# Performance work log

Measured on AMD Instinct MI355X. Metric: run time of the kernel, lower is better.

## Reference

```python
import jax, jax.numpy as jnp
import numpy as np

B, D, P = 8192, 256, 4096
TEMP = 0.5
MOMENTUM = 0.9
EPS = 1e-12  # matches torch F.normalize eps


def _l2_normalize(x):
    n = jnp.sqrt(jnp.sum(x * x, axis=1, keepdims=True))
    return x / jnp.maximum(n, EPS)


def setup_inputs() -> dict:
    key = jax.random.key(0)
    k1, k2, k3 = jax.random.split(key, 3)
    embeddings = jax.random.normal(k1, (B, D), dtype=jnp.float32)
    prototypes = jax.random.normal(k2, (P, D), dtype=jnp.float32)
    cluster_ids = jax.random.randint(k3, (B,), 0, P, dtype=jnp.int64)
    return {"embeddings": embeddings, "prototypes": prototypes, "cluster_ids": cluster_ids}


def reference(embeddings, prototypes, cluster_ids):
    cluster_ids = cluster_ids.astype(jnp.int32)
    emb_norm = _l2_normalize(embeddings)            # [B, D]
    proto_norm = _l2_normalize(prototypes)          # [P, D]
    sim = (emb_norm @ proto_norm.T) / TEMP          # [B, P]

    rows = jnp.arange(sim.shape[0])
    pos_sim = sim[rows, cluster_ids]                # [B]
    neg_sim = sim.at[rows, cluster_ids].set(-jnp.inf)
    # stable logsumexp over negatives (positive column masked out)
    max_val = jnp.max(neg_sim, axis=1, keepdims=True)
    lse = jnp.log(jnp.sum(jnp.exp(neg_sim - max_val), axis=1)) + max_val[:, 0]
    loss = jnp.mean(-pos_sim + lse)

    # serial per-sample EMA prototype update (faithful to the torch for-loop,
    # including sequential dependence on repeated cluster ids)
    def step(protos, xe):
        cid, e = xe
        new_row = MOMENTUM * protos[cid] + (1.0 - MOMENTUM) * e
        return protos.at[cid].set(new_row), None

    new_prototypes, _ = jax.lax.scan(step, prototypes, (cluster_ids, embeddings))
    return loss, new_prototypes
```

## Files before the change

kernel.cpp:

```cpp
#include <hip/hip_runtime.h>
#include <hip/hip_bf16.h>
#include <math.h>

#define Bn 8192
#define Dn 256
#define Pn 4096

#define SCALE 2.8853900817779268f
#define LN2   0.6931471805599453f

using f16x8 = _Float16 __attribute__((ext_vector_type(8)));
using f16x4 = _Float16 __attribute__((ext_vector_type(4)));
using f32x16 = float __attribute__((ext_vector_type(16)));

__global__ void norm_hist_kernel(const float* __restrict__ emb, const float* __restrict__ protos,
                                 const int* __restrict__ cid,
                                 _Float16* __restrict__ embn, _Float16* __restrict__ pron,
                                 float* __restrict__ s_glob, int* __restrict__ hist) {
    __shared__ int h[Pn];
    int gid  = blockIdx.x;
    bool do_hist = (gid < Bn / 256);
    if (do_hist)
        for (int c = threadIdx.x; c < Pn; c += 256) h[c] = 0;

    int row  = gid * 4 + (threadIdx.x >> 6);
    int lane = threadIdx.x & 63;
    const float* in;
    _Float16* out;
    int r;
    float post;
    if (row < Bn) { in = emb;    out = embn; r = row;      post = SCALE; }
    else          { in = protos; out = pron; r = row - Bn; post = 1.0f;  }
    const float4 v = reinterpret_cast<const float4*>(in + (size_t)r * Dn)[lane];
    float ss = v.x * v.x + v.y * v.y + v.z * v.z + v.w * v.w;
#pragma unroll
    for (int m = 1; m <= 32; m <<= 1) ss += __shfl_xor(ss, m);
    float scale = post / fmaxf(sqrtf(ss), 1e-12f);
    f16x4 o;
    o[0] = (_Float16)(v.x * scale);
    o[1] = (_Float16)(v.y * scale);
    o[2] = (_Float16)(v.z * scale);
    o[3] = (_Float16)(v.w * scale);
    reinterpret_cast<f16x4*>(out + (size_t)r * Dn)[lane] = o;

    if (gid < 32) s_glob[gid * 256 + threadIdx.x] = 0.0f;

    if (do_hist) {
        __syncthreads();
        atomicAdd(&h[cid[gid * 256 + threadIdx.x]], 1);
        __syncthreads();
        for (int c = threadIdx.x; c < Pn; c += 256)
            hist[gid * Pn + c] = h[c];
    }
}

__global__ __launch_bounds__(256, 2)
void gemm_expsum_kernel(const _Float16* __restrict__ embn, const _Float16* __restrict__ pron,
                        float* __restrict__ s_glob) {
    __shared__ _Float16 Bs[2][32 * Dn];
    const int w    = threadIdx.x >> 6;
    const int lane = threadIdx.x & 63;
    const int lo   = lane & 31;
    const int hi   = lane >> 5;
    const int rbase = blockIdx.x * 128 + w * 32;
    const int cbase = blockIdx.y * 256;

    const _Float16* ap = embn + (size_t)(rbase + lo) * Dn + hi * 8;
    f16x8 a[16];
#pragma unroll
    for (int kk = 0; kk < 16; ++kk)
        a[kk] = *reinterpret_cast<const f16x8*>(ap + kk * 16);

    float s[16];
#pragma unroll
    for (int r = 0; r < 16; ++r) s[r] = 0.0f;

    auto stage = [&](int sub, _Float16* buf) {
#pragma unroll
        for (int i = 0; i < 4; ++i) {
            int g = i * 4 + w;
            const _Float16* gsrc =
                pron + (size_t)(cbase + sub * 32 + lo) * Dn + g * 16 + hi * 8;
            char* l = (char*)buf + (g << 10);
            __builtin_amdgcn_global_load_lds(
                (const __attribute__((address_space(1))) unsigned int*)gsrc,
                (__attribute__((address_space(3))) unsigned int*)l, 16, 0, 0);
        }
    };

    stage(0, Bs[0]);
    __syncthreads();

    for (int sub = 0; sub < 8; ++sub) {
        const _Float16* cur = Bs[sub & 1];
        if (sub < 7) stage(sub + 1, Bs[(sub + 1) & 1]);

        f32x16 acc;
#pragma unroll
        for (int r = 0; r < 16; ++r) acc[r] = 0.0f;
#pragma unroll
        for (int kk = 0; kk < 16; ++kk) {
            f16x8 b = *reinterpret_cast<const f16x8*>(
                (const char*)cur + (kk << 10) + (lane << 4));
            acc = __builtin_amdgcn_mfma_f32_32x32x16_f16(a[kk], b, acc, 0, 0, 0);
        }
#pragma unroll
        for (int r = 0; r < 16; ++r)
            s[r] += __builtin_amdgcn_exp2f(acc[r]);

        __syncthreads();
    }

#pragma unroll
    for (int r = 0; r < 16; ++r) {
        float v = s[r];
        v += __shfl_xor(v, 1);
        v += __shfl_xor(v, 2);
        v += __shfl_xor(v, 4);
        v += __shfl_xor(v, 8);
        v += __shfl_xor(v, 16);
        if (lo == 0) {
            int row = rbase + (r & 3) + 8 * (r >> 2) + 4 * hi;
            atomicAdd(&s_glob[row], v);
        }
    }
}

__global__ void loss_terms_kernel(const _Float16* __restrict__ embn, const _Float16* __restrict__ pron,
                                  const int* __restrict__ cid, const float* __restrict__ s_glob,
                                  float* __restrict__ terms) {
    int row  = blockIdx.x * 4 + (threadIdx.x >> 6);
    int lane = threadIdx.x & 63;
    int c = cid[row];
    f16x4 e = reinterpret_cast<const f16x4*>(embn + (size_t)row * Dn)[lane];
    f16x4 p = reinterpret_cast<const f16x4*>(pron + (size_t)c * Dn)[lane];
    float d = 0.0f;
#pragma unroll
    for (int j = 0; j < 4; ++j) d += (float)e[j] * (float)p[j];
#pragma unroll
    for (int m = 1; m <= 32; m <<= 1) d += __shfl_xor(d, m);
    if (lane == 0) {
        float accp = d;
        float sneg = s_glob[row] - __builtin_amdgcn_exp2f(accp);
        terms[row] = __logf(sneg) - LN2 * accp;
    }
}

__global__ void counts_pref_kernel(const int* __restrict__ hist, int* __restrict__ counts,
                                   int* __restrict__ pref) {
    int c = blockIdx.x * 256 + threadIdx.x;
    int s = 0;
#pragma unroll
    for (int ch = 0; ch < 32; ++ch) {
        pref[ch * Pn + c] = s;
        s += hist[ch * Pn + c];
    }
    counts[c] = s;
}

__global__ void offsets_kernel(const int* __restrict__ counts, int* __restrict__ offs) {
    __shared__ int wtot[4];
    int t = threadIdx.x;
    int local[16];
    int run = 0;
#pragma unroll
    for (int j = 0; j < 16; ++j) { local[j] = run; run += counts[t * 16 + j]; }
    int v = run;
#pragma unroll
    for (int d = 1; d < 64; d <<= 1) {
        int u = __shfl_up(v, d);
        if ((t & 63) >= d) v += u;
    }
    if ((t & 63) == 63) wtot[t >> 6] = v;
    __syncthreads();
    int add = 0;
    for (int ww = 0; ww < (t >> 6); ++ww) add += wtot[ww];
    int excl = add + v - run;
#pragma unroll
    for (int j = 0; j < 16; ++j) offs[t * 16 + j] = excl + local[j];
    if (t == 0) offs[Pn] = Bn;
}

__global__ void rankfill_kernel(const int* __restrict__ cid, const int* __restrict__ pref,
                                const int* __restrict__ offs, int* __restrict__ slist) {
    __shared__ int ids[256];
    int t = threadIdx.x, g = blockIdx.x;
    int i = g * 256 + t;
    int my = cid[i];
    ids[t] = my;
    __syncthreads();
    int r = pref[g * Pn + my];
    for (int j = 0; j < t; ++j) r += (ids[j] == my) ? 1 : 0;
    slist[offs[my] + r] = i;
}

__global__ void update_loss_kernel(const float* __restrict__ protos, const float* __restrict__ emb,
                                   const int* __restrict__ offs, const int* __restrict__ slist,
                                   const float* __restrict__ terms, float* __restrict__ out) {
    __shared__ float ws2[4];
    float* outp = out + 1;
    int w = threadIdx.x >> 6, lane = threadIdx.x & 63;
    int c = blockIdx.x * 4 + w;
    int off = offs[c], cnt = offs[c + 1] - off;
    float4 p = reinterpret_cast<const float4*>(protos + (size_t)c * Dn)[lane];
    float scale = __powf(0.9f, (float)cnt);
    float4 acc;
    acc.x = p.x * scale; acc.y = p.y * scale; acc.z = p.z * scale; acc.w = p.w * scale;
    for (int j = 0; j < cnt; ++j) {
        int i = slist[off + j];
        float wgt = 0.1f * __powf(0.9f, (float)(cnt - 1 - j));
        float4 e = reinterpret_cast<const float4*>(emb + (size_t)i * Dn)[lane];
        acc.x += wgt * e.x; acc.y += wgt * e.y; acc.z += wgt * e.z; acc.w += wgt * e.w;
    }
    reinterpret_cast<float4*>(outp + (size_t)c * Dn)[lane] = acc;

    if (blockIdx.x == 0) {
        float ssum = 0.0f;
        for (int i = threadIdx.x; i < Bn; i += 256) ssum += terms[i];
#pragma unroll
        for (int m = 1; m <= 32; m <<= 1) ssum += __shfl_xor(ssum, m);
        if ((threadIdx.x & 63) == 0) ws2[threadIdx.x >> 6] = ssum;
        __syncthreads();
        if (threadIdx.x == 0)
            out[0] = (ws2[0] + ws2[1] + ws2[2] + ws2[3]) * (1.0f / (float)Bn);
    }
}

extern "C" void kernel_launch(void* const* d_in, const int* in_sizes, int n_in,
                              void* d_out, int out_size, void* d_ws, size_t ws_size,
                              hipStream_t stream) {
    const float* emb    = (const float*)d_in[0];
    const float* protos = (const float*)d_in[1];
    const int*   cid    = (const int*)d_in[2];
    float* out = (float*)d_out;

    char* ws = (char*)d_ws;
    _Float16* embn = (_Float16*)ws;
    _Float16* pron = (_Float16*)(ws + ((size_t)4 << 20));
    float* s_glob  = (float*)(ws + ((size_t)6 << 20));
    float* terms   = (float*)(ws + ((size_t)6 << 20) + 32768);
    int*   offs    = (int*)(ws + ((size_t)6 << 20) + 65536);
    int*   slist   = (int*)(ws + ((size_t)6 << 20) + 98304);
    int*   counts  = (int*)(ws + ((size_t)6 << 20) + 131072);
    int*   hist    = (int*)(ws + ((size_t)7 << 20));
    int*   pref    = (int*)(ws + ((size_t)7 << 20) + 524288);

    norm_hist_kernel<<<(Bn + Pn) / 4, 256, 0, stream>>>(emb, protos, cid, embn, pron, s_glob, hist);
    gemm_expsum_kernel<<<dim3(Bn / 128, Pn / 256), 256, 0, stream>>>(embn, pron, s_glob);
    loss_terms_kernel<<<Bn / 4, 256, 0, stream>>>(embn, pron, cid, s_glob, terms);
    counts_pref_kernel<<<Pn / 256, 256, 0, stream>>>(hist, counts, pref);
    offsets_kernel<<<1, 256, 0, stream>>>(counts, offs);
    rankfill_kernel<<<Bn / 256, 256, 0, stream>>>(cid, pref, offs, slist);
    update_loss_kernel<<<Pn / 4, 256, 0, stream>>>(protos, emb, offs, slist, terms, out);
}
```

Baseline: 126.2 us.

## Switch GEMM-expsum to 16x16x32 MFMA tiles with smaller row blocks

The similarity GEMM now uses 16x16x32 MFMA instructions instead of 32x32x16. Each wave handles 16 rows against two 16-column tiles per 32-column stage. The block covers 64 rows instead of 128, which doubles the grid and raises launch_bounds occupancy from 2 to 4 blocks per SM. This cuts per-thread registers (A fragments and accumulators), so more waves can be resident to hide latency. The cost is that each staged prototype tile is reused by fewer rows, so global and LDS traffic for prototypes doubles, and there are more atomics.

```diff
diff --git a/kernel.cpp b/kernel.cpp
--- a/kernel.cpp
+++ b/kernel.cpp
@@ -11,7 +11,7 @@
 
 using f16x8 = _Float16 __attribute__((ext_vector_type(8)));
 using f16x4 = _Float16 __attribute__((ext_vector_type(4)));
-using f32x16 = float __attribute__((ext_vector_type(16)));
+using f32x4 = float __attribute__((ext_vector_type(4)));
 
 __global__ void norm_hist_kernel(const float* __restrict__ emb, const float* __restrict__ protos,
                                  const int* __restrict__ cid,
@@ -54,33 +54,34 @@
     }
 }
 
-__global__ __launch_bounds__(256, 2)
+__global__ __launch_bounds__(256, 4)
 void gemm_expsum_kernel(const _Float16* __restrict__ embn, const _Float16* __restrict__ pron,
                         float* __restrict__ s_glob) {
     __shared__ _Float16 Bs[2][32 * Dn];
     const int w    = threadIdx.x >> 6;
     const int lane = threadIdx.x & 63;
-    const int lo   = lane & 31;
-    const int hi   = lane >> 5;
-    const int rbase = blockIdx.x * 128 + w * 32;
+    const int c16  = lane & 15;
+    const int q    = lane >> 4;
+    const int rbase = blockIdx.x * 64 + w * 16;
     const int cbase = blockIdx.y * 256;
 
-    const _Float16* ap = embn + (size_t)(rbase + lo) * Dn + hi * 8;
-    f16x8 a[16];
-#pragma unroll
-    for (int kk = 0; kk < 16; ++kk)
-        a[kk] = *reinterpret_cast<const f16x8*>(ap + kk * 16);
-
-    float s[16];
-#pragma unroll
-    for (int r = 0; r < 16; ++r) s[r] = 0.0f;
+    const _Float16* ap = embn + (size_t)(rbase + c16) * Dn + q * 8;
+    f16x8 a[8];
+#pragma unroll
+    for (int kk = 0; kk < 8; ++kk)
+        a[kk] = *reinterpret_cast<const f16x8*>(ap + kk * 32);
+
+    float s[4];
+#pragma unroll
+    for (int r = 0; r < 4; ++r) s[r] = 0.0f;
 
     auto stage = [&](int sub, _Float16* buf) {
 #pragma unroll
         for (int i = 0; i < 4; ++i) {
-            int g = i * 4 + w;
+            int g  = i * 4 + w;
+            int ct = g >> 3, kk = g & 7;
             const _Float16* gsrc =
-                pron + (size_t)(cbase + sub * 32 + lo) * Dn + g * 16 + hi * 8;
+                pron + (size_t)(cbase + sub * 32 + ct * 16 + c16) * Dn + kk * 32 + q * 8;
             char* l = (char*)buf + (g << 10);
             __builtin_amdgcn_global_load_lds(
                 (const __attribute__((address_space(1))) unsigned int*)gsrc,
@@ -92,37 +93,34 @@
     __syncthreads();
 
     for (int sub = 0; sub < 8; ++sub) {
-        const _Float16* cur = Bs[sub & 1];
+        const char* cur = (const char*)Bs[sub & 1];
         if (sub < 7) stage(sub + 1, Bs[(sub + 1) & 1]);
 
-        f32x16 acc;
-#pragma unroll
-        for (int r = 0; r < 16; ++r) acc[r] = 0.0f;
-#pragma unroll
-        for (int kk = 0; kk < 16; ++kk) {
-            f16x8 b = *reinterpret_cast<const f16x8*>(
-                (const char*)cur + (kk << 10) + (lane << 4));
-            acc = __builtin_amdgcn_mfma_f32_32x32x16_f16(a[kk], b, acc, 0, 0, 0);
+        f32x4 acc0 = {0.0f, 0.0f, 0.0f, 0.0f};
+        f32x4 acc1 = {0.0f, 0.0f, 0.0f, 0.0f};
+#pragma unroll
+        for (int kk = 0; kk < 8; ++kk) {
+            f16x8 b0 = *reinterpret_cast<const f16x8*>(cur + (kk << 10) + (lane << 4));
+            acc0 = __builtin_amdgcn_mfma_f32_16x16x32_f16(a[kk], b0, acc0, 0, 0, 0);
+            f16x8 b1 = *reinterpret_cast<const f16x8*>(cur + ((8 + kk) << 10) + (lane << 4));
+            acc1 = __builtin_amdgcn_mfma_f32_16x16x32_f16(a[kk], b1, acc1, 0, 0, 0);
         }
 #pragma unroll
-        for (int r = 0; r < 16; ++r)
-            s[r] += __builtin_amdgcn_exp2f(acc[r]);
-
-        __syncthreads();
-    }
-
-#pragma unroll
-    for (int r = 0; r < 16; ++r) {
+        for (int r = 0; r < 4; ++r)
+            s[r] += __builtin_amdgcn_exp2f(acc0[r]) + __builtin_amdgcn_exp2f(acc1[r]);
+
+        __syncthreads();
+    }
+
+#pragma unroll
+    for (int r = 0; r < 4; ++r) {
         float v = s[r];
         v += __shfl_xor(v, 1);
         v += __shfl_xor(v, 2);
         v += __shfl_xor(v, 4);
         v += __shfl_xor(v, 8);
-        v += __shfl_xor(v, 16);
-        if (lo == 0) {
-            int row = rbase + (r & 3) + 8 * (r >> 2) + 4 * hi;
-            atomicAdd(&s_glob[row], v);
-        }
+        if (c16 == 0)
+            atomicAdd(&s_glob[rbase + q * 4 + r], v);
     }
 }
 
@@ -246,7 +244,7 @@
     int*   pref    = (int*)(ws + ((size_t)7 << 20) + 524288);
 
     norm_hist_kernel<<<(Bn + Pn) / 4, 256, 0, stream>>>(emb, protos, cid, embn, pron, s_glob, hist);
-    gemm_expsum_kernel<<<dim3(Bn / 128, Pn / 256), 256, 0, stream>>>(embn, pron, s_glob);
+    gemm_expsum_kernel<<<dim3(Bn / 64, Pn / 256), 256, 0, stream>>>(embn, pron, s_glob);
     loss_terms_kernel<<<Bn / 4, 256, 0, stream>>>(embn, pron, cid, s_glob, terms);
     counts_pref_kernel<<<Pn / 256, 256, 0, stream>>>(hist, counts, pref);
     offsets_kernel<<<1, 256, 0, stream>>>(counts, offs);
```

New measurement: 132.6 us. +5.0%, slower.
